# Kernel tuning notes

Measured on AMD Instinct MI355X. Metric: run time of the kernel, lower is better.

## Reference

```python
import jax, jax.numpy as jnp
import numpy as np

C = 2048   # in_channels (= inter_channels, nhead=1)
H, W = 8, 4
L = H * W  # 32 pseudo-tokens
N = 32     # detections (queries)
M = 16     # tracklets (gallery)


def _conv1x1(t, w, b=None):
    # t: [P, C, H, W], w: [Cout, Cin]
    y = jnp.einsum('oc,pchw->pohw', w, t)
    if b is not None:
        y = y + b[None, :, None, None]
    return y


def _layernorm(t, w, b, eps=1e-5):
    # torch LayerNorm over normalized_shape=[C, 8, 4] -> last 3 axes
    mu = t.mean(axis=(1, 2, 3), keepdims=True)
    var = t.var(axis=(1, 2, 3), keepdims=True)
    return (t - mu) / jnp.sqrt(var + eps) * w[None] + b[None]


def setup_inputs():
    key = jax.random.key(0)
    ks = jax.random.split(key, 16)
    s = 0.02
    return {
        'x':    jax.random.normal(ks[0], (N, C, H, W), jnp.float32),
        'x_g':  jax.random.normal(ks[1], (M, C, H, W), jnp.float32),
        'Wq': jax.random.normal(ks[2], (C, C), jnp.float32) * s,
        'bq': jnp.zeros((C,), jnp.float32),
        'Wk': jax.random.normal(ks[3], (C, C), jnp.float32) * s,
        'bk': jnp.zeros((C,), jnp.float32),
        'Wv': jax.random.normal(ks[4], (C, C), jnp.float32) * s,
        'bv': jnp.zeros((C,), jnp.float32),
        'Wo': jax.random.normal(ks[5], (C, C), jnp.float32) * s,
        'bo': jnp.zeros((C,), jnp.float32),
        'W1': jax.random.normal(ks[6], (C, C), jnp.float32) * s,  # conv1, bias=False
        'W2': jax.random.normal(ks[7], (C, C), jnp.float32) * s,  # conv2, bias=False
        'ln1_w': jnp.ones((C, H, W), jnp.float32),
        'ln1_b': jnp.zeros((C, H, W), jnp.float32),
        'ln2_w': jnp.ones((C, H, W), jnp.float32),
        'ln2_b': jnp.zeros((C, H, W), jnp.float32),
    }


def reference(x, x_g, Wq, bq, Wk, bk, Wv, bv, Wo, bo, W1, W2, ln1_w, ln1_b, ln2_w, ln2_b):
    n, m = x.shape[0], x_g.shape[0]
    # torch.where(ones((m, n)) > 0): row-major -> gallery idx repeats, query idx tiles
    gs = jnp.repeat(jnp.arange(m), n)
    qs = jnp.tile(jnp.arange(n), m)
    xp = x[qs]      # [P, C, H, W] per-pair query features
    xg = x_g[gs]    # [P, C, H, W] per-pair gallery features
    P = n * m

    # Faithful to torch: conv output [P,C,H,W] -> .view(P, -1, C) scrambles
    # channel/spatial into L pseudo-tokens of width C (row-major reshape).
    q = _conv1x1(xg, Wq, bq).reshape(P, L, C)
    k = _conv1x1(xp, Wk, bk).reshape(P, L, C)
    v = _conv1x1(xp, Wv, bv).reshape(P, L, C)

    # nhead=1 -> head dim of size 1; scale = sqrt(k.shape[2]) = sqrt(L)
    scores = jnp.einsum('plc,pmc->plm', q, k)[:, None] / np.sqrt(L)  # [P,1,L,L]
    # Faithful to torch Softmax(dim=1): softmax over the head dim (size 1)
    attn = jax.nn.softmax(scores, axis=1)
    att = jnp.einsum('pnlm,pmc->pnlc', attn, v)          # [P,1,L,C]
    att = jnp.swapaxes(att.reshape(P, L, C), 1, 2)       # [P,C,L]
    att = att.reshape(P, C, H, W)
    att = _conv1x1(att, Wo, bo)

    # scatter_add over query index
    agg = jax.ops.segment_sum(att, qs, num_segments=n)   # [N,C,H,W]

    h1 = agg + x                      # res1 (dropout1 = 0)
    h1 = _layernorm(h1, ln1_w, ln1_b) # norm1
    h2 = _conv1x1(jax.nn.relu(_conv1x1(h1, W1)), W2)  # mlp, dropouts = 0
    out = h1 + h2                     # res2
    out = _layernorm(out, ln2_w, ln2_b)
    return out
```

## Files before the change

kernel.cpp:

```cpp
#include <hip/hip_runtime.h>

typedef unsigned short u16;
typedef unsigned int u32;
typedef unsigned long long u64;
typedef __attribute__((ext_vector_type(8))) short bf16x8;
typedef __attribute__((ext_vector_type(4))) float f32x4;

#define CCH 2048

__device__ __forceinline__ u16 f2bf(float f) {
    unsigned int x = __float_as_uint(f);
    unsigned int r = (x + 0x7fffu + ((x >> 16) & 1u)) >> 16;
    return (u16)r;
}

__device__ __forceinline__ void gload_lds16(const u16* g, u16* l) {
    __builtin_amdgcn_global_load_lds((const __attribute__((address_space(1))) void*)g,
                                     (__attribute__((address_space(3))) void*)l, 16, 0, 0);
}

__global__ void k_convert3(const float* __restrict__ W1, const float* __restrict__ W2,
                           const float* __restrict__ Wo,
                           u16* __restrict__ W1b, u16* __restrict__ W2b, u16* __restrict__ Wob) {
    long tg = (long)blockIdx.x * 256 + threadIdx.x;
    long base = tg * 4;
    const float* src; u16* dst; long off;
    if (base < 4194304)      { src = W1; dst = W1b; off = base; }
    else if (base < 8388608) { src = W2; dst = W2b; off = base - 4194304; }
    else                     { src = Wo; dst = Wob; off = base - 8388608; }
    float4 v = *(const float4*)&src[off];
    u64 p = (u64)f2bf(v.x) | ((u64)f2bf(v.y) << 16) | ((u64)f2bf(v.z) << 32) | ((u64)f2bf(v.w) << 48);
    *(u64*)&dst[off] = p;
}

__global__ void k_wvsum(const float* __restrict__ Wv, const float* __restrict__ bv,
                        u16* __restrict__ WvSumb, float* __restrict__ bvSum) {
    int t = blockIdx.x * 256 + threadIdx.x;
    int j = t >> 11;
    float s = 0.f;
    #pragma unroll 8
    for (int m = 0; m < 32; ++m) s += Wv[(m * 64 + j) * CCH + (t & 2047)];
    WvSumb[t] = f2bf(s);
    if (t < 64) {
        float b = 0.f;
        for (int m = 0; m < 32; ++m) b += bv[m * 64 + t];
        bvSum[t] = b;
    }
}

__global__ void k_xpose(const float* __restrict__ x, u16* __restrict__ xTb) {
    int cb = blockIdx.x, q = blockIdx.y;
    int t = threadIdx.x;
    int c0 = cb * 64;
    __shared__ float ftile[32][33];
    u32* xT32 = (u32*)xTb;
    #pragma unroll
    for (int half = 0; half < 2; ++half) {
        int ch = c0 + half * 32;
        #pragma unroll
        for (int k = 0; k < 4; ++k) {
            int i = t + k * 256;
            ftile[i & 31][i >> 5] = x[q * 65536 + (ch + (i >> 5)) * 32 + (i & 31)];
        }
        __syncthreads();
        #pragma unroll
        for (int k = 0; k < 2; ++k) {
            int i = t + k * 256;
            int s = i >> 4, cp = i & 15;
            u32 val = (u32)f2bf(ftile[s][cp * 2]) | ((u32)f2bf(ftile[s][cp * 2 + 1]) << 16);
            xT32[(size_t)(q * 32 + s) * 1024 + (ch >> 1) + cp] = val;
        }
        __syncthreads();
    }
}

__global__ __launch_bounds__(256) void k_sv_gemm(const u16* __restrict__ A, const u16* __restrict__ B,
                                                 float* __restrict__ P) {
    int n0 = blockIdx.x * 64;
    int kc = blockIdx.y;
    int t = threadIdx.x;
    int lane = t & 63, wid = t >> 6;
    int wm = wid * 16;
    int l15 = lane & 15, lhi = lane >> 4, sw = l15 & 7;
    int offk[2] = { ((lhi) ^ sw) * 8, ((4 + lhi) ^ sw) * 8 };
    __shared__ u16 At[2][64 * 64];
    __shared__ u16 Bt[2][64 * 64];
    f32x4 z = {0.f, 0.f, 0.f, 0.f};
    f32x4 acc[4] = {z, z, z, z};
    int srow = t >> 3, scol = ((t & 7) ^ (srow & 7)) * 8;
    int kbase = kc * 512;

    auto STAGE = [&](int p, int k0) {
        #pragma unroll
        for (int i = 0; i < 2; ++i) {
            gload_lds16(A + (size_t)(i * 32 + srow) * CCH + k0 + scol, &At[p][i * 2048 + t * 8]);
            gload_lds16(B + (size_t)(n0 + i * 32 + srow) * CCH + k0 + scol, &Bt[p][i * 2048 + t * 8]);
        }
    };
    STAGE(0, kbase);
    __syncthreads();
    int cur = 0;
    for (int kt = 0; kt < 8; ++kt) {
        if (kt < 7) STAGE(cur ^ 1, kbase + (kt + 1) * 64);
        #pragma unroll
        for (int ks = 0; ks < 2; ++ks) {
            bf16x8 af = *(const bf16x8*)&At[cur][(wm + l15) * 64 + offk[ks]];
            #pragma unroll
            for (int fn = 0; fn < 4; ++fn) {
                bf16x8 bf = *(const bf16x8*)&Bt[cur][(fn * 16 + l15) * 64 + offk[ks]];
                acc[fn] = __builtin_amdgcn_mfma_f32_16x16x32_bf16(af, bf, acc[fn], 0, 0, 0);
            }
        }
        __syncthreads();
        cur ^= 1;
    }
    #pragma unroll
    for (int fn = 0; fn < 4; ++fn)
        #pragma unroll
        for (int r = 0; r < 4; ++r) {
            int j = wm + lhi * 4 + r;
            int col = n0 + fn * 16 + l15;
            P[kc * 65536 + j * 1024 + col] = acc[fn][r];
        }
}

__global__ void k_sv_reduce(const float* __restrict__ P, const float* __restrict__ bvSum,
                            u16* __restrict__ Svb) {
    int idx0 = blockIdx.x * 1024 + threadIdx.x;
    #pragma unroll
    for (int k = 0; k < 4; ++k) {
        int idx = idx0 + k * 256;
        int j = idx >> 10, col = idx & 1023;
        float v = bvSum[j];
        #pragma unroll
        for (int kc = 0; kc < 4; ++kc) v += P[kc * 65536 + idx];
        Svb[(size_t)(col >> 5) * CCH + j * 32 + (col & 31)] = f2bf(v);
    }
}

__global__ __launch_bounds__(256) void k_t_gemm(const u16* __restrict__ A, const u16* __restrict__ B,
                                                float* __restrict__ P) {
    int m0 = blockIdx.x * 128;
    int kc = blockIdx.y;
    int t = threadIdx.x;
    int lane = t & 63, wid = t >> 6;
    int wm = wid * 32;
    int l15 = lane & 15, lhi = lane >> 4, sw = l15 & 7;
    int offk[2] = { ((lhi) ^ sw) * 8, ((4 + lhi) ^ sw) * 8 };
    __shared__ u16 At[2][128 * 64];
    __shared__ u16 Bt[2][32 * 64];
    f32x4 z = {0.f, 0.f, 0.f, 0.f};
    f32x4 acc[2][2] = {{z, z}, {z, z}};
    int srow = t >> 3, scol = ((t & 7) ^ (srow & 7)) * 8;
    int kbase = kc * 512;

    auto STAGE = [&](int p, int k0) {
        #pragma unroll
        for (int i = 0; i < 4; ++i)
            gload_lds16(A + (size_t)(m0 + i * 32 + srow) * CCH + k0 + scol, &At[p][i * 2048 + t * 8]);
        gload_lds16(B + (size_t)srow * CCH + k0 + scol, &Bt[p][t * 8]);
    };
    STAGE(0, kbase);
    __syncthreads();
    int cur = 0;
    for (int kt = 0; kt < 8; ++kt) {
        if (kt < 7) STAGE(cur ^ 1, kbase + (kt + 1) * 64);
        #pragma unroll
        for (int ks = 0; ks < 2; ++ks) {
            bf16x8 af[2], bf[2];
            #pragma unroll
            for (int fm = 0; fm < 2; ++fm)
                af[fm] = *(const bf16x8*)&At[cur][(wm + fm * 16 + l15) * 64 + offk[ks]];
            #pragma unroll
            for (int fn = 0; fn < 2; ++fn)
                bf[fn] = *(const bf16x8*)&Bt[cur][(fn * 16 + l15) * 64 + offk[ks]];
            #pragma unroll
            for (int fm = 0; fm < 2; ++fm)
                #pragma unroll
                for (int fn = 0; fn < 2; ++fn)
                    acc[fm][fn] = __builtin_amdgcn_mfma_f32_16x16x32_bf16(af[fm], bf[fn], acc[fm][fn], 0, 0, 0);
        }
        __syncthreads();
        cur ^= 1;
    }
    #pragma unroll
    for (int fm = 0; fm < 2; ++fm)
        #pragma unroll
        for (int fn = 0; fn < 2; ++fn)
            #pragma unroll
            for (int r = 0; r < 4; ++r) {
                int mg = m0 + wm + fm * 16 + lhi * 4 + r;
                int cg = fn * 16 + l15;
                P[kc * 65536 + mg * 32 + cg] = acc[fm][fn][r];
            }
}

__global__ void k_t_reduce(const float* __restrict__ P, const float* __restrict__ bo,
                           float* __restrict__ Tm) {
    int idx0 = blockIdx.x * 1024 + threadIdx.x;
    #pragma unroll
    for (int k = 0; k < 4; ++k) {
        int idx = idx0 + k * 256;
        int q = idx >> 11, o = idx & 2047;
        float v = bo[o];
        #pragma unroll
        for (int kc = 0; kc < 4; ++kc) v += P[kc * 65536 + o * 32 + q];
        Tm[q * CCH + o] = v;
    }
}

__global__ void k_ln1stat(const float* __restrict__ Tm, const float* __restrict__ x,
                          float* __restrict__ p1, float* __restrict__ p2) {
    int q = blockIdx.x, ch = blockIdx.y;
    int t = threadIdx.x;
    float sum = 0.f, ssq = 0.f;
    for (int j = 0; j < 32; ++j) {
        int i = ch * 8192 + j * 256 + t;
        float v = 16.f * Tm[q * CCH + (i >> 5)] + x[q * 65536 + i];
        sum += v; ssq += v * v;
    }
    #pragma unroll
    for (int off = 32; off > 0; off >>= 1) {
        sum += __shfl_down(sum, off);
        ssq += __shfl_down(ssq, off);
    }
    __shared__ float rs[4], rq[4];
    if ((t & 63) == 0) { rs[t >> 6] = sum; rq[t >> 6] = ssq; }
    __syncthreads();
    if (t == 0) {
        p1[q * 8 + ch] = rs[0] + rs[1] + rs[2] + rs[3];
        p2[q * 8 + ch] = rq[0] + rq[1] + rq[2] + rq[3];
    }
}

__global__ void k_lnfinish(const float* __restrict__ p1, const float* __restrict__ p2,
                           float* __restrict__ stats) {
    int q = blockIdx.x;
    if (threadIdx.x == 0) {
        float S = 0.f, Q = 0.f;
        for (int c = 0; c < 8; ++c) { S += p1[q * 8 + c]; Q += p2[q * 8 + c]; }
        float mu = S * (1.f / 65536.f);
        float var = Q * (1.f / 65536.f) - mu * mu;
        stats[q * 2] = mu;
        stats[q * 2 + 1] = rsqrtf(var + 1e-5f);
    }
}

__global__ void k_ln1apply(const float* __restrict__ Tm, const float* __restrict__ x,
                           const float* __restrict__ stats,
                           const float* __restrict__ lnw, const float* __restrict__ lnb,
                           float* __restrict__ h1, u16* __restrict__ h1b) {
    int q = blockIdx.x, cb = blockIdx.y;
    int t = threadIdx.x;
    float mu = stats[q * 2], rstd = stats[q * 2 + 1];
    __shared__ u16 tile[32 * 132];
    for (int j = 0; j < 16; ++j) {
        int i = cb * 4096 + j * 256 + t;
        float v = 16.f * Tm[q * CCH + (i >> 5)] + x[q * 65536 + i];
        float g = (v - mu) * rstd * lnw[i] + lnb[i];
        h1[q * 65536 + i] = g;
        int cl = (j * 256 + t) >> 5;
        tile[(i & 31) * 132 + cl] = f2bf(g);
    }
    __syncthreads();
    for (int j = 0; j < 16; ++j) {
        int idx = j * 256 + t;
        int s = idx >> 7, cl = idx & 127;
        h1b[(size_t)(q * 32 + s) * CCH + cb * 128 + cl] = tile[s * 132 + cl];
    }
}

__global__ __launch_bounds__(256) void k_mfma_gemm_sk(
        const u16* __restrict__ A, const u16* __restrict__ B,
        float* __restrict__ P, int ldc) {
    int m0 = blockIdx.x * 128;
    int n0 = blockIdx.y * 64;
    int kc = blockIdx.z;
    int t = threadIdx.x;
    int lane = t & 63, wid = t >> 6;
    int wm = (wid >> 1) * 64, wn = (wid & 1) * 32;
    int l15 = lane & 15, lhi = lane >> 4, sw = l15 & 7;
    int offk[2] = { ((lhi) ^ sw) * 8, ((4 + lhi) ^ sw) * 8 };

    __shared__ u16 Atile[2][128 * 64];
    __shared__ u16 Btile[2][64 * 64];

    f32x4 z = {0.f, 0.f, 0.f, 0.f};
    f32x4 acc[4][2] = {{z, z}, {z, z}, {z, z}, {z, z}};

    int srow = t >> 3;
    int scol = ((t & 7) ^ (srow & 7)) * 8;
    int kbase = kc * 1024;

    auto STAGE = [&](int p, int k0) {
        #pragma unroll
        for (int i = 0; i < 4; ++i)
            gload_lds16(A + (size_t)(m0 + i * 32 + srow) * CCH + k0 + scol,
                        &Atile[p][i * 2048 + t * 8]);
        #pragma unroll
        for (int i = 0; i < 2; ++i)
            gload_lds16(B + (size_t)(n0 + i * 32 + srow) * CCH + k0 + scol,
                        &Btile[p][i * 2048 + t * 8]);
    };

    STAGE(0, kbase);
    __syncthreads();
    int cur = 0;
    for (int kt = 0; kt < 16; ++kt) {
        if (kt < 15) STAGE(cur ^ 1, kbase + (kt + 1) * 64);
        #pragma unroll
        for (int ks = 0; ks < 2; ++ks) {
            bf16x8 af[4], bf[2];
            #pragma unroll
            for (int fm = 0; fm < 4; ++fm)
                af[fm] = *(const bf16x8*)&Atile[cur][(wm + fm * 16 + l15) * 64 + offk[ks]];
            #pragma unroll
            for (int fn = 0; fn < 2; ++fn)
                bf[fn] = *(const bf16x8*)&Btile[cur][(wn + fn * 16 + l15) * 64 + offk[ks]];
            #pragma unroll
            for (int fm = 0; fm < 4; ++fm)
                #pragma unroll
                for (int fn = 0; fn < 2; ++fn)
                    acc[fm][fn] = __builtin_amdgcn_mfma_f32_16x16x32_bf16(
                        af[fm], bf[fn], acc[fm][fn], 0, 0, 0);
        }
        __syncthreads();
        cur ^= 1;
    }

    #pragma unroll
    for (int fm = 0; fm < 4; ++fm)
        #pragma unroll
        for (int fn = 0; fn < 2; ++fn)
            #pragma unroll
            for (int r = 0; r < 4; ++r) {
                int mg = m0 + wm + fm * 16 + lhi * 4 + r;
                int cg = n0 + wn + fn * 16 + l15;
                P[(size_t)kc * 2097152 + (size_t)mg * ldc + cg] = acc[fm][fn][r];
            }
}

__global__ void k_g1_reduce(const float* __restrict__ P, u16* __restrict__ Y1b) {
    int idx = (blockIdx.x * 256 + threadIdx.x) * 4;
    float4 a = *(const float4*)&P[idx];
    float4 b = *(const float4*)&P[2097152 + idx];
    u64 p = (u64)f2bf(fmaxf(a.x + b.x, 0.f))
          | ((u64)f2bf(fmaxf(a.y + b.y, 0.f)) << 16)
          | ((u64)f2bf(fmaxf(a.z + b.z, 0.f)) << 32)
          | ((u64)f2bf(fmaxf(a.w + b.w, 0.f)) << 48);
    *(u64*)&Y1b[idx] = p;
}

__global__ void k_g2_reduce(const float* __restrict__ P, const float* __restrict__ h1,
                            float* __restrict__ out) {
    int idx = (blockIdx.x * 256 + threadIdx.x) * 4;
    int o = idx >> 10, tok = idx & 1023;
    int q = tok >> 5, s = tok & 31;
    size_t oaddr = (size_t)q * 65536 + (size_t)o * 32 + s;
    float4 a = *(const float4*)&P[idx];
    float4 b = *(const float4*)&P[2097152 + idx];
    float4 h = *(const float4*)&h1[oaddr];
    float4 v;
    v.x = a.x + b.x + h.x; v.y = a.y + b.y + h.y;
    v.z = a.z + b.z + h.z; v.w = a.w + b.w + h.w;
    *(float4*)&out[oaddr] = v;
}

__global__ void k_ln2stat(const float* __restrict__ io,
                          float* __restrict__ p1, float* __restrict__ p2) {
    int q = blockIdx.x, ch = blockIdx.y;
    int t = threadIdx.x;
    float sum = 0.f, ssq = 0.f;
    for (int j = 0; j < 32; ++j) {
        float v = io[q * 65536 + ch * 8192 + j * 256 + t];
        sum += v; ssq += v * v;
    }
    #pragma unroll
    for (int off = 32; off > 0; off >>= 1) {
        sum += __shfl_down(sum, off);
        ssq += __shfl_down(ssq, off);
    }
    __shared__ float rs[4], rq[4];
    if ((t & 63) == 0) { rs[t >> 6] = sum; rq[t >> 6] = ssq; }
    __syncthreads();
    if (t == 0) {
        p1[q * 8 + ch] = rs[0] + rs[1] + rs[2] + rs[3];
        p2[q * 8 + ch] = rq[0] + rq[1] + rq[2] + rq[3];
    }
}

__global__ void k_ln2apply(float* __restrict__ io, const float* __restrict__ stats,
                           const float* __restrict__ lnw, const float* __restrict__ lnb) {
    int q = blockIdx.x, cb = blockIdx.y;
    int t = threadIdx.x;
    float mu = stats[q * 2], rstd = stats[q * 2 + 1];
    for (int j = 0; j < 16; ++j) {
        int i = cb * 4096 + j * 256 + t;
        float v = io[q * 65536 + i];
        io[q * 65536 + i] = (v - mu) * rstd * lnw[i] + lnb[i];
    }
}

extern "C" void kernel_launch(void* const* d_in, const int* in_sizes, int n_in,
                              void* d_out, int out_size, void* d_ws, size_t ws_size,
                              hipStream_t stream) {
    const float* x    = (const float*)d_in[0];
    const float* Wv   = (const float*)d_in[6];
    const float* bv   = (const float*)d_in[7];
    const float* Wo   = (const float*)d_in[8];
    const float* bo   = (const float*)d_in[9];
    const float* W1   = (const float*)d_in[10];
    const float* W2   = (const float*)d_in[11];
    const float* ln1w = (const float*)d_in[12];
    const float* ln1b = (const float*)d_in[13];
    const float* ln2w = (const float*)d_in[14];
    const float* ln2b = (const float*)d_in[15];
    float* out = (float*)d_out;

    float* ws    = (float*)d_ws;
    float* bvSum = ws;
    float* stats = ws + 64;
    float* p1    = ws + 128;
    float* p2    = ws + 384;
    float* Psv   = ws + 640;
    float* Pt    = ws + 262784;
    float* Tm    = ws + 524928;
    float* h1    = ws + 590464;
    float* Pg    = ws + 2687616;
    u16* ub      = (u16*)(ws + 6881920);
    u16* WvSumb  = ub;
    u16* xTb     = ub + 131072;
    u16* Svb     = ub + 2228224;
    u16* h1b     = ub + 2293760;
    u16* Y1b     = ub + 4390912;
    u16* W1b     = ub + 6488064;
    u16* W2b     = ub + 10682368;
    u16* Wob     = ub + 14876672;

    k_convert3<<<12288, 256, 0, stream>>>(W1, W2, Wo, W1b, W2b, Wob);
    k_wvsum<<<512, 256, 0, stream>>>(Wv, bv, WvSumb, bvSum);
    k_xpose<<<dim3(32, 32), 256, 0, stream>>>(x, xTb);
    k_sv_gemm<<<dim3(16, 4), 256, 0, stream>>>(WvSumb, xTb, Psv);
    k_sv_reduce<<<64, 256, 0, stream>>>(Psv, bvSum, Svb);
    k_t_gemm<<<dim3(16, 4), 256, 0, stream>>>(Wob, Svb, Pt);
    k_t_reduce<<<64, 256, 0, stream>>>(Pt, bo, Tm);
    k_ln1stat<<<dim3(32, 8), 256, 0, stream>>>(Tm, x, p1, p2);
    k_lnfinish<<<32, 64, 0, stream>>>(p1, p2, stats);
    k_ln1apply<<<dim3(32, 16), 256, 0, stream>>>(Tm, x, stats, ln1w, ln1b, h1, h1b);
    k_mfma_gemm_sk<<<dim3(8, 32, 2), 256, 0, stream>>>(h1b, W1b, Pg, 2048);
    k_g1_reduce<<<2048, 256, 0, stream>>>(Pg, Y1b);
    k_mfma_gemm_sk<<<dim3(16, 16, 2), 256, 0, stream>>>(W2b, Y1b, Pg, 1024);
    k_g2_reduce<<<2048, 256, 0, stream>>>(Pg, h1, out);
    k_ln2stat<<<dim3(32, 8), 256, 0, stream>>>(out, p1, p2);
    k_lnfinish<<<32, 64, 0, stream>>>(p1, p2, stats);
    k_ln2apply<<<dim3(32, 16), 256, 0, stream>>>(out, stats, ln2w, ln2b);
}
```

Before: 114.2 us.

## Fuse prep kernels and merge reductions with layernorm statistics passes

Merges the three weight/input preparation kernels into one launch, folds the T reduction into the LN1 statistics kernel, folds the GEMM2 split-K reduction into the LN2 statistics kernel, and removes the lnfinish kernels by recomputing mean and rstd inside the apply kernels. This cuts the launch count from 17 to 11 and removes the round trips for re-reading Tm and out. In exchange, the fused g2 kernel gives each thread one channel row of 32 contiguous floats, so a wavefront's accesses are strided across rows rather than fully coalesced. Each apply thread also redundantly sums the partial statistics.

```diff
diff --git a/kernel.cpp b/kernel.cpp
--- a/kernel.cpp
+++ b/kernel.cpp
@@ -19,58 +19,60 @@
                                      (__attribute__((address_space(3))) void*)l, 16, 0, 0);
 }
 
-__global__ void k_convert3(const float* __restrict__ W1, const float* __restrict__ W2,
-                           const float* __restrict__ Wo,
-                           u16* __restrict__ W1b, u16* __restrict__ W2b, u16* __restrict__ Wob) {
-    long tg = (long)blockIdx.x * 256 + threadIdx.x;
-    long base = tg * 4;
-    const float* src; u16* dst; long off;
-    if (base < 4194304)      { src = W1; dst = W1b; off = base; }
-    else if (base < 8388608) { src = W2; dst = W2b; off = base - 4194304; }
-    else                     { src = Wo; dst = Wob; off = base - 8388608; }
-    float4 v = *(const float4*)&src[off];
-    u64 p = (u64)f2bf(v.x) | ((u64)f2bf(v.y) << 16) | ((u64)f2bf(v.z) << 32) | ((u64)f2bf(v.w) << 48);
-    *(u64*)&dst[off] = p;
-}
-
-__global__ void k_wvsum(const float* __restrict__ Wv, const float* __restrict__ bv,
-                        u16* __restrict__ WvSumb, float* __restrict__ bvSum) {
-    int t = blockIdx.x * 256 + threadIdx.x;
-    int j = t >> 11;
-    float s = 0.f;
-    #pragma unroll 8
-    for (int m = 0; m < 32; ++m) s += Wv[(m * 64 + j) * CCH + (t & 2047)];
-    WvSumb[t] = f2bf(s);
-    if (t < 64) {
-        float b = 0.f;
-        for (int m = 0; m < 32; ++m) b += bv[m * 64 + t];
-        bvSum[t] = b;
-    }
-}
-
-__global__ void k_xpose(const float* __restrict__ x, u16* __restrict__ xTb) {
-    int cb = blockIdx.x, q = blockIdx.y;
-    int t = threadIdx.x;
-    int c0 = cb * 64;
+__global__ void k_prep(const float* __restrict__ W1, const float* __restrict__ W2,
+                       const float* __restrict__ Wo, const float* __restrict__ Wv,
+                       const float* __restrict__ bv, const float* __restrict__ x,
+                       u16* __restrict__ W1b, u16* __restrict__ W2b, u16* __restrict__ Wob,
+                       u16* __restrict__ WvSumb, float* __restrict__ bvSum,
+                       u16* __restrict__ xTb) {
+    int b = blockIdx.x;
+    int t = threadIdx.x;
     __shared__ float ftile[32][33];
-    u32* xT32 = (u32*)xTb;
-    #pragma unroll
-    for (int half = 0; half < 2; ++half) {
-        int ch = c0 + half * 32;
-        #pragma unroll
-        for (int k = 0; k < 4; ++k) {
-            int i = t + k * 256;
-            ftile[i & 31][i >> 5] = x[q * 65536 + (ch + (i >> 5)) * 32 + (i & 31)];
-        }
-        __syncthreads();
-        #pragma unroll
-        for (int k = 0; k < 2; ++k) {
-            int i = t + k * 256;
-            int s = i >> 4, cp = i & 15;
-            u32 val = (u32)f2bf(ftile[s][cp * 2]) | ((u32)f2bf(ftile[s][cp * 2 + 1]) << 16);
-            xT32[(size_t)(q * 32 + s) * 1024 + (ch >> 1) + cp] = val;
-        }
-        __syncthreads();
+    if (b < 12288) {
+        long base = (long)b * 1024 + t * 4;
+        const float* src; u16* dst; long off;
+        if (base < 4194304)      { src = W1; dst = W1b; off = base; }
+        else if (base < 8388608) { src = W2; dst = W2b; off = base - 4194304; }
+        else                     { src = Wo; dst = Wob; off = base - 8388608; }
+        float4 v = *(const float4*)&src[off];
+        u64 p = (u64)f2bf(v.x) | ((u64)f2bf(v.y) << 16)
+              | ((u64)f2bf(v.z) << 32) | ((u64)f2bf(v.w) << 48);
+        *(u64*)&dst[off] = p;
+    } else if (b < 12800) {
+        int tt = (b - 12288) * 256 + t;
+        int j = tt >> 11;
+        float s = 0.f;
+        #pragma unroll 8
+        for (int m = 0; m < 32; ++m) s += Wv[(m * 64 + j) * CCH + (tt & 2047)];
+        WvSumb[tt] = f2bf(s);
+        if (tt < 64) {
+            float bb = 0.f;
+            for (int m = 0; m < 32; ++m) bb += bv[m * 64 + tt];
+            bvSum[tt] = bb;
+        }
+    } else {
+        int bb = b - 12800;
+        int cb = bb & 31, q = bb >> 5;
+        int c0 = cb * 64;
+        u32* xT32 = (u32*)xTb;
+        #pragma unroll
+        for (int half = 0; half < 2; ++half) {
+            int ch = c0 + half * 32;
+            #pragma unroll
+            for (int k = 0; k < 4; ++k) {
+                int i = t + k * 256;
+                ftile[i & 31][i >> 5] = x[q * 65536 + (ch + (i >> 5)) * 32 + (i & 31)];
+            }
+            __syncthreads();
+            #pragma unroll
+            for (int k = 0; k < 2; ++k) {
+                int i = t + k * 256;
+                int s = i >> 4, cp = i & 15;
+                u32 val = (u32)f2bf(ftile[s][cp * 2]) | ((u32)f2bf(ftile[s][cp * 2 + 1]) << 16);
+                xT32[(size_t)(q * 32 + s) * 1024 + (ch >> 1) + cp] = val;
+            }
+            __syncthreads();
+        }
     }
 }
 
@@ -195,29 +197,25 @@
             }
 }
 
-__global__ void k_t_reduce(const float* __restrict__ P, const float* __restrict__ bo,
-                           float* __restrict__ Tm) {
-    int idx0 = blockIdx.x * 1024 + threadIdx.x;
-    #pragma unroll
-    for (int k = 0; k < 4; ++k) {
-        int idx = idx0 + k * 256;
-        int q = idx >> 11, o = idx & 2047;
-        float v = bo[o];
-        #pragma unroll
-        for (int kc = 0; kc < 4; ++kc) v += P[kc * 65536 + o * 32 + q];
-        Tm[q * CCH + o] = v;
-    }
-}
-
-__global__ void k_ln1stat(const float* __restrict__ Tm, const float* __restrict__ x,
-                          float* __restrict__ p1, float* __restrict__ p2) {
+__global__ void k_t_reduce_ln1(const float* __restrict__ P, const float* __restrict__ bo,
+                               const float* __restrict__ x, float* __restrict__ Tm,
+                               float* __restrict__ p1, float* __restrict__ p2) {
     int q = blockIdx.x, ch = blockIdx.y;
     int t = threadIdx.x;
+    int c = ch * 256 + t;
+    float T = bo[c];
+    #pragma unroll
+    for (int kc = 0; kc < 4; ++kc) T += P[kc * 65536 + c * 32 + q];
+    Tm[q * CCH + c] = T;
+    float T16 = 16.f * T;
+    const float* xr = x + (size_t)q * 65536 + (size_t)c * 32;
     float sum = 0.f, ssq = 0.f;
-    for (int j = 0; j < 32; ++j) {
-        int i = ch * 8192 + j * 256 + t;
-        float v = 16.f * Tm[q * CCH + (i >> 5)] + x[q * 65536 + i];
-        sum += v; ssq += v * v;
+    #pragma unroll
+    for (int s4 = 0; s4 < 8; ++s4) {
+        float4 xv = *(const float4*)&xr[s4 * 4];
+        float v0 = T16 + xv.x, v1 = T16 + xv.y, v2 = T16 + xv.z, v3 = T16 + xv.w;
+        sum += v0 + v1 + v2 + v3;
+        ssq += v0 * v0 + v1 * v1 + v2 * v2 + v3 * v3;
     }
     #pragma unroll
     for (int off = 32; off > 0; off >>= 1) {
@@ -233,26 +231,17 @@
     }
 }
 
-__global__ void k_lnfinish(const float* __restrict__ p1, const float* __restrict__ p2,
-                           float* __restrict__ stats) {
-    int q = blockIdx.x;
-    if (threadIdx.x == 0) {
-        float S = 0.f, Q = 0.f;
-        for (int c = 0; c < 8; ++c) { S += p1[q * 8 + c]; Q += p2[q * 8 + c]; }
-        float mu = S * (1.f / 65536.f);
-        float var = Q * (1.f / 65536.f) - mu * mu;
-        stats[q * 2] = mu;
-        stats[q * 2 + 1] = rsqrtf(var + 1e-5f);
-    }
-}
-
 __global__ void k_ln1apply(const float* __restrict__ Tm, const float* __restrict__ x,
-                           const float* __restrict__ stats,
+                           const float* __restrict__ p1, const float* __restrict__ p2,
                            const float* __restrict__ lnw, const float* __restrict__ lnb,
                            float* __restrict__ h1, u16* __restrict__ h1b) {
     int q = blockIdx.x, cb = blockIdx.y;
     int t = threadIdx.x;
-    float mu = stats[q * 2], rstd = stats[q * 2 + 1];
+    float S = 0.f, Q = 0.f;
+    #pragma unroll
+    for (int cch = 0; cch < 8; ++cch) { S += p1[q * 8 + cch]; Q += p2[q * 8 + cch]; }
+    float mu = S * (1.f / 65536.f);
+    float rstd = rsqrtf(Q * (1.f / 65536.f) - mu * mu + 1e-5f);
     __shared__ u16 tile[32 * 132];
     for (int j = 0; j < 16; ++j) {
         int i = cb * 4096 + j * 256 + t;
@@ -351,29 +340,27 @@
     *(u64*)&Y1b[idx] = p;
 }
 
-__global__ void k_g2_reduce(const float* __restrict__ P, const float* __restrict__ h1,
-                            float* __restrict__ out) {
-    int idx = (blockIdx.x * 256 + threadIdx.x) * 4;
-    int o = idx >> 10, tok = idx & 1023;
-    int q = tok >> 5, s = tok & 31;
-    size_t oaddr = (size_t)q * 65536 + (size_t)o * 32 + s;
-    float4 a = *(const float4*)&P[idx];
-    float4 b = *(const float4*)&P[2097152 + idx];
-    float4 h = *(const float4*)&h1[oaddr];
-    float4 v;
-    v.x = a.x + b.x + h.x; v.y = a.y + b.y + h.y;
-    v.z = a.z + b.z + h.z; v.w = a.w + b.w + h.w;
-    *(float4*)&out[oaddr] = v;
-}
-
-__global__ void k_ln2stat(const float* __restrict__ io,
-                          float* __restrict__ p1, float* __restrict__ p2) {
+__global__ void k_g2_ln2(const float* __restrict__ P, const float* __restrict__ h1,
+                         float* __restrict__ out, float* __restrict__ p1, float* __restrict__ p2) {
     int q = blockIdx.x, ch = blockIdx.y;
     int t = threadIdx.x;
+    int o = ch * 256 + t;
+    const float* P0 = P + (size_t)o * 1024 + q * 32;
+    const float* P1 = P + 2097152 + (size_t)o * 1024 + q * 32;
+    const float* hr = h1 + (size_t)q * 65536 + (size_t)o * 32;
+    float* orow = out + (size_t)q * 65536 + (size_t)o * 32;
     float sum = 0.f, ssq = 0.f;
-    for (int j = 0; j < 32; ++j) {
-        float v = io[q * 65536 + ch * 8192 + j * 256 + t];
-        sum += v; ssq += v * v;
+    #pragma unroll
+    for (int s4 = 0; s4 < 8; ++s4) {
+        float4 a = *(const float4*)&P0[s4 * 4];
+        float4 b = *(const float4*)&P1[s4 * 4];
+        float4 h = *(const float4*)&hr[s4 * 4];
+        float4 v;
+        v.x = a.x + b.x + h.x; v.y = a.y + b.y + h.y;
+        v.z = a.z + b.z + h.z; v.w = a.w + b.w + h.w;
+        *(float4*)&orow[s4 * 4] = v;
+        sum += v.x + v.y + v.z + v.w;
+        ssq += v.x * v.x + v.y * v.y + v.z * v.z + v.w * v.w;
     }
     #pragma unroll
     for (int off = 32; off > 0; off >>= 1) {
@@ -389,11 +376,16 @@
     }
 }
 
-__global__ void k_ln2apply(float* __restrict__ io, const float* __restrict__ stats,
+__global__ void k_ln2apply(float* __restrict__ io, const float* __restrict__ p1,
+                           const float* __restrict__ p2,
                            const float* __restrict__ lnw, const float* __restrict__ lnb) {
     int q = blockIdx.x, cb = blockIdx.y;
     int t = threadIdx.x;
-    float mu = stats[q * 2], rstd = stats[q * 2 + 1];
+    float S = 0.f, Q = 0.f;
+    #pragma unroll
+    for (int cch = 0; cch < 8; ++cch) { S += p1[q * 8 + cch]; Q += p2[q * 8 + cch]; }
+    float mu = S * (1.f / 65536.f);
+    float rstd = rsqrtf(Q * (1.f / 65536.f) - mu * mu + 1e-5f);
     for (int j = 0; j < 16; ++j) {
         int i = cb * 4096 + j * 256 + t;
         float v = io[q * 65536 + i];
@@ -419,7 +411,6 @@
 
     float* ws    = (float*)d_ws;
     float* bvSum = ws;
-    float* stats = ws + 64;
     float* p1    = ws + 128;
     float* p2    = ws + 384;
     float* Psv   = ws + 640;
@@ -437,21 +428,15 @@
     u16* W2b     = ub + 10682368;
     u16* Wob     = ub + 14876672;
 
-    k_convert3<<<12288, 256, 0, stream>>>(W1, W2, Wo, W1b, W2b, Wob);
-    k_wvsum<<<512, 256, 0, stream>>>(Wv, bv, WvSumb, bvSum);
-    k_xpose<<<dim3(32, 32), 256, 0, stream>>>(x, xTb);
+    k_prep<<<13824, 256, 0, stream>>>(W1, W2, Wo, Wv, bv, x, W1b, W2b, Wob, WvSumb, bvSum, xTb);
     k_sv_gemm<<<dim3(16, 4), 256, 0, stream>>>(WvSumb, xTb, Psv);
     k_sv_reduce<<<64, 256, 0, stream>>>(Psv, bvSum, Svb);
     k_t_gemm<<<dim3(16, 4), 256, 0, stream>>>(Wob, Svb, Pt);
-    k_t_reduce<<<64, 256, 0, stream>>>(Pt, bo, Tm);
-    k_ln1stat<<<dim3(32, 8), 256, 0, stream>>>(Tm, x, p1, p2);
-    k_lnfinish<<<32, 64, 0, stream>>>(p1, p2, stats);
-    k_ln1apply<<<dim3(32, 16), 256, 0, stream>>>(Tm, x, stats, ln1w, ln1b, h1, h1b);
+    k_t_reduce_ln1<<<dim3(32, 8), 256, 0, stream>>>(Pt, bo, x, Tm, p1, p2);
+    k_ln1apply<<<dim3(32, 16), 256, 0, stream>>>(Tm, x, p1, p2, ln1w, ln1b, h1, h1b);
     k_mfma_gemm_sk<<<dim3(8, 32, 2), 256, 0, stream>>>(h1b, W1b, Pg, 2048);
     k_g1_reduce<<<2048, 256, 0, stream>>>(Pg, Y1b);
     k_mfma_gemm_sk<<<dim3(16, 16, 2), 256, 0, stream>>>(W2b, Y1b, Pg, 1024);
-    k_g2_reduce<<<2048, 256, 0, stream>>>(Pg, h1, out);
-    k_ln2stat<<<dim3(32, 8), 256, 0, stream>>>(out, p1, p2);
-    k_lnfinish<<<32, 64, 0, stream>>>(p1, p2, stats);
-    k_ln2apply<<<dim3(32, 16), 256, 0, stream>>>(out, stats, ln2w, ln2b);
-}
+    k_g2_ln2<<<dim3(32, 8), 256, 0, stream>>>(Pg, h1, out, p1, p2);
+    k_ln2apply<<<dim3(32, 16), 256, 0, stream>>>(out, p1, p2, ln2w, ln2b);
+}
```

Result: faster. 107.8 us (-5.6%).
